# Optimization experiments

Hardware: AMD Instinct MI355X
Metric: run time of the kernel (lower is better)

Reference implementation:

```python
import jax, jax.numpy as jnp
import numpy as np

TEMP = 0.07  # temperature used as logits / 0.07 in the original


def setup_inputs() -> dict:
    key = jax.random.key(0)
    k1, k2, k3 = jax.random.split(key, 3)
    B, N, T, L, D = 8, 128, 8, 6, 256
    meta = jax.random.normal(k1, (B, N, T, L, D), dtype=jnp.float32)
    thing = jax.random.randint(k2, (B, N, T), 0, 2, dtype=jnp.int32)
    label = jax.random.randint(k3, (B, N, T), 0, 40, dtype=jnp.int32)
    return {"meta_weight_for_con": meta, "thing_gt_idx": thing, "label_tmp": label}


def _con_loss(meta, thing, label):
    # meta: [B,N,T,L,D]; thing,label: [B,N,T]
    B, N, T, L, D = meta.shape
    P = N * T
    valid = thing.reshape(B, P).astype(bool)            # [B,P] boolean gt mask
    lab = label.reshape(B, P)                           # [B,P]
    # meta_weight_b[mask] -> [K,L,D]; permute(1,0,2) -> per-layer [K,D].
    # We keep all P positions and mask instead of compacting (jit-friendly).
    w = meta.reshape(B, P, L, D).transpose(0, 2, 1, 3)  # [B,L,P,D]
    w = w / jnp.maximum(jnp.linalg.norm(w, axis=-1, keepdims=True), 1e-12)  # F.normalize
    z = jnp.einsum('blpd,blqd->blpq', w, w) / TEMP      # similarity / temp [B,L,P,P]

    same = lab[:, :, None] == lab[:, None, :]           # [B,P,P]
    vpair = valid[:, :, None] & valid[:, None, :]
    eye = jnp.eye(P, dtype=bool)
    pos_mask = same & (~eye) & vpair                    # positives: same label, not self
    neg_mask = (~same) & vpair                          # negatives: different label

    K = valid.sum(axis=1)                               # [B] ins_num_ per batch
    pos_count = pos_mask.sum(axis=-1)                   # [B,P]
    neg_count = neg_mask.sum(axis=-1)                   # [B,P]

    # --- random positive sample per (batch, layer, row), mirroring np.random.choice ---
    u = jax.random.uniform(jax.random.key(42), (B, L, P))
    r = jnp.floor(u * pos_count[:, None, :].astype(u.dtype)).astype(jnp.int32)
    r = jnp.minimum(r, jnp.maximum(pos_count - 1, 0)[:, None, :])
    ranks = jnp.cumsum(pos_mask, axis=-1) - 1           # rank of each positive in index order
    sel = pos_mask[:, None, :, :] & (ranks[:, None, :, :] == r[..., None])  # [B,L,P,P]
    zp = jnp.sum(jnp.where(sel, z, 0.0), axis=-1)       # chosen positive logit [B,L,P]
    diag = jnp.diagonal(z, axis1=-2, axis2=-1)          # self-sim fallback when no positives
    zp = jnp.where((pos_count > 0)[:, None, :], zp, diag)

    # --- last negative (original pads by repeating the last negative to K-1) ---
    iota = jnp.arange(P)
    idx_last = jnp.max(jnp.where(neg_mask, iota[None, None, :], -1), axis=-1)  # [B,P]
    idx = jnp.broadcast_to(jnp.maximum(idx_last, 0)[:, None, :, None], (B, L, P, 1))
    zl = jnp.take_along_axis(z, idx, axis=-1)[..., 0]   # [B,L,P]

    # --- stable CE with label 0: loss = lse(logits) - zp ---
    max_n = jnp.max(jnp.where(neg_mask[:, None], z, -jnp.inf), axis=-1)  # [B,L,P]
    m = jnp.maximum(zp, max_n)
    m = jnp.where(jnp.isfinite(m), m, zp)
    sum_neg = jnp.sum(jnp.where(neg_mask[:, None], jnp.exp(z - m[..., None]), 0.0), axis=-1)
    pad = jnp.maximum((K[:, None] - 1 - neg_count), 0).astype(z.dtype)   # [B,P]
    pad_term = pad[:, None, :] * jnp.where((neg_count > 0)[:, None, :], jnp.exp(zl - m), 0.0)
    loss_row = m + jnp.log(jnp.exp(zp - m) + sum_neg + pad_term) - zp    # [B,L,P]

    row_w = valid.astype(z.dtype)
    mean_per = jnp.sum(loss_row * row_w[:, None, :], axis=-1) / jnp.maximum(K, 1)[:, None].astype(z.dtype)  # [B,L]

    gate = jnp.sum((thing.sum(axis=2) > 0), axis=1) >= 2  # skip batches with <2 gt rows
    return jnp.sum(jnp.where(gate[:, None], mean_per, 0.0))


def reference(meta_weight_for_con, thing_gt_idx, label_tmp):
    return _con_loss(meta_weight_for_con, thing_gt_idx, label_tmp)
```

## Files before the change

### kernel.cpp

```cpp
#include <hip/hip_runtime.h>
#include <stdint.h>

namespace {

constexpr int Bb = 8, Ll = 6, Dd = 256, Pp = 1024;
constexpr float SCALE_Y = 14.285714285714286f * 1.4426950408889634f;
constexpr float M0y = 21.0f;
constexpr float LN2f = 0.6931471805599453f;

typedef __attribute__((ext_vector_type(4))) float floatx4;

__device__ const int PAIRS[36] = {
  0x00,0x01,0x02,0x03,0x04,0x05,0x06,0x07,
  0x11,0x12,0x13,0x14,0x15,0x16,0x17,
  0x22,0x23,0x24,0x25,0x26,0x27,
  0x33,0x34,0x35,0x36,0x37,
  0x44,0x45,0x46,0x47,
  0x55,0x56,0x57,
  0x66,0x67,
  0x77
};

__device__ __forceinline__ void async16(const void* g, void* l) {
  __builtin_amdgcn_global_load_lds(
      (const __attribute__((address_space(1))) void*)g,
      (__attribute__((address_space(3))) void*)l, 16, 0, 0);
}

__device__ __forceinline__ uint32_t rotl32(uint32_t x, int n) {
  return (x << n) | (x >> (32 - n));
}
__device__ __forceinline__ void tf_round(uint32_t& x0, uint32_t& x1, int r) {
  x0 += x1; x1 = rotl32(x1, r); x1 ^= x0;
}
__device__ void threefry2x32(uint32_t x0, uint32_t x1, uint32_t& o0, uint32_t& o1) {
  const uint32_t k0 = 0u, k1 = 42u;
  const uint32_t k2 = k0 ^ k1 ^ 0x1BD11BDAu;
  x0 += k0; x1 += k1;
  tf_round(x0,x1,13); tf_round(x0,x1,15); tf_round(x0,x1,26); tf_round(x0,x1,6);
  x0 += k1; x1 += k2 + 1u;
  tf_round(x0,x1,17); tf_round(x0,x1,29); tf_round(x0,x1,16); tf_round(x0,x1,24);
  x0 += k2; x1 += k0 + 2u;
  tf_round(x0,x1,13); tf_round(x0,x1,15); tf_round(x0,x1,26); tf_round(x0,x1,6);
  x0 += k0; x1 += k1 + 3u;
  tf_round(x0,x1,17); tf_round(x0,x1,29); tf_round(x0,x1,16); tf_round(x0,x1,24);
  x0 += k1; x1 += k2 + 4u;
  tf_round(x0,x1,13); tf_round(x0,x1,15); tf_round(x0,x1,26); tf_round(x0,x1,6);
  x0 += k2; x1 += k0 + 5u;
  o0 = x0; o1 = x1;
}
__device__ float jax_u01(uint32_t idx) {
  const uint32_t HALF = (uint32_t)(Bb * Ll * Pp / 2);
  uint32_t o0, o1, bits;
  if (idx < HALF) { threefry2x32(idx, idx + HALF, o0, o1); bits = o0; }
  else            { threefry2x32(idx - HALF, idx, o0, o1); bits = o1; }
  return __uint_as_float((bits >> 9) | 0x3f800000u) - 1.0f;
}

__device__ __forceinline__ uint32_t fp8e4m3_rne(float x) {
  uint32_t u = __float_as_uint(x);
  const uint32_t s = (u >> 24) & 0x80u;
  u &= 0x7FFFFFFFu;
  uint32_t code;
  if (u < 0x3C800000u) {
    code = (uint32_t)__float2int_rn(__uint_as_float(u) * 512.0f);
  } else {
    const uint32_t r = (u + 0x7FFFFu + ((u >> 20) & 1u)) >> 20;
    code = r - (120u << 3);
  }
  return s | code;
}
__device__ __forceinline__ float fp8e4m3_tof(uint32_t c) {
  const uint32_t e = (c >> 3) & 15u, m = c & 7u;
  float mag;
  if (e) mag = __uint_as_float(((e + 120u) << 23) | (m << 20));
  else   mag = (float)m * 0.001953125f;
  return (c & 0x80u) ? -mag : mag;
}

__device__ __forceinline__ void fp8x4_dot(uint32_t a, uint32_t b, float& s) {
#if __has_builtin(__builtin_amdgcn_cvt_f32_fp8)
  s += __builtin_amdgcn_cvt_f32_fp8((int)a, 0) * __builtin_amdgcn_cvt_f32_fp8((int)b, 0);
  s += __builtin_amdgcn_cvt_f32_fp8((int)a, 1) * __builtin_amdgcn_cvt_f32_fp8((int)b, 1);
  s += __builtin_amdgcn_cvt_f32_fp8((int)a, 2) * __builtin_amdgcn_cvt_f32_fp8((int)b, 2);
  s += __builtin_amdgcn_cvt_f32_fp8((int)a, 3) * __builtin_amdgcn_cvt_f32_fp8((int)b, 3);
#else
  s += fp8e4m3_tof(a & 0xFF) * fp8e4m3_tof(b & 0xFF);
  s += fp8e4m3_tof((a >> 8) & 0xFF) * fp8e4m3_tof((b >> 8) & 0xFF);
  s += fp8e4m3_tof((a >> 16) & 0xFF) * fp8e4m3_tof((b >> 16) & 0xFF);
  s += fp8e4m3_tof((a >> 24) & 0xFF) * fp8e4m3_tof((b >> 24) & 0xFF);
#endif
}

constexpr int NB_NORM = Bb * Pp * Ll / 4;
constexpr int NB_ROW  = Bb * Pp / 4;

__global__ void prep_k(const float* __restrict__ meta, const int* __restrict__ thing,
                       const int* __restrict__ label, uint8_t* __restrict__ wn,
                       int* __restrict__ qpos, int* __restrict__ negc,
                       int* __restrict__ qidx, int* __restrict__ Kv,
                       int* __restrict__ gatev, float* __restrict__ rowsum_g,
                       int* __restrict__ cnt2, float* __restrict__ out) {
  __shared__ int sK[256], sG[256];
  const int bid = blockIdx.x, t = threadIdx.x;

  if (bid < NB_NORM) {
    const int wid = (bid * 256 + t) >> 6;
    const int lane = t & 63;
    const float4 v = *(const float4*)(meta + (size_t)wid * Dd + lane * 4);
    float ss = v.x * v.x + v.y * v.y + v.z * v.z + v.w * v.w;
    #pragma unroll
    for (int m = 32; m; m >>= 1) ss += __shfl_xor(ss, m, 64);
    const float inv = 1.0f / fmaxf(sqrtf(ss), 1e-12f);
    const int bp = wid / Ll, l = wid - bp * Ll;
    const int b = bp >> 10, p = bp & (Pp - 1);
    uint8_t* dst = wn + ((size_t)(b * Ll + l) * Pp + p) * Dd + lane * 4;
#if __has_builtin(__builtin_amdgcn_cvt_pk_fp8_f32)
    const int lo16 = __builtin_amdgcn_cvt_pk_fp8_f32(v.x * inv, v.y * inv, 0, false);
    const uint32_t packed =
        (uint32_t)__builtin_amdgcn_cvt_pk_fp8_f32(v.z * inv, v.w * inv, lo16, true);
#else
    const uint32_t packed = fp8e4m3_rne(v.x * inv)
                          | (fp8e4m3_rne(v.y * inv) << 8)
                          | (fp8e4m3_rne(v.z * inv) << 16)
                          | (fp8e4m3_rne(v.w * inv) << 24);
#endif
    *(uint32_t*)dst = packed;
    return;
  }
  if (bid < NB_NORM + NB_ROW) {
    const int wid = (bid - NB_NORM) * 4 + (t >> 6);
    const int lane = t & 63;
    const int b = wid >> 10, p = wid & (Pp - 1);
    const int* lab = label + b * Pp;
    const int* th  = thing + b * Pp;
    const int myLab = lab[p];
    const bool myValid = (th[p] != 0);

    uint32_t posbits = 0;
    int cnt[16];
    int pc = 0, nc = 0, last = -1;
    #pragma unroll
    for (int c = 0; c < 16; ++c) {
      const int q = c * 64 + lane;
      const int lq = lab[q];
      const bool vq = (th[q] != 0);
      const bool same = (lq == myLab);
      const bool pos = myValid && vq && same && (q != p);
      const bool neg = myValid && vq && !same;
      uint64_t bp2 = __ballot(pos);
      uint64_t bn = __ballot(neg);
      if (pos) posbits |= (1u << c);
      cnt[c] = __popcll(bp2);
      pc += cnt[c];
      nc += __popcll(bn);
      if (bn) last = c * 64 + 63 - __clzll(bn);
    }
    int qsel[Ll];
    #pragma unroll
    for (int l = 0; l < Ll; ++l) qsel[l] = p;
    if (pc > 0) {
      for (int l = 0; l < Ll; ++l) {
        const float u = jax_u01((uint32_t)((b * Ll + l) * Pp + p));
        int r = (int)floorf(u * (float)pc);
        r = min(r, pc - 1);
        int base = 0;
        for (int c = 0; c < 16; ++c) {
          if (r < base + cnt[c]) {
            const bool mine = (posbits >> c) & 1u;
            uint64_t bm = __ballot(mine);
            uint64_t ltmask = (lane == 0) ? 0ull : (~0ull >> (64 - lane));
            int myrank = __popcll(bm & ltmask);
            bool hit = mine && (base + myrank == r);
            uint64_t hb = __ballot(hit);
            qsel[l] = c * 64 + (int)__builtin_ctzll(hb);
            break;
          }
          base += cnt[c];
        }
      }
    }
    if (lane == 0) {
      negc[wid] = nc;
      qidx[wid] = (last < 0) ? 0 : last;
      #pragma unroll
      for (int l = 0; l < Ll; ++l) qpos[(b * Ll + l) * Pp + p] = qsel[l];
    }
    return;
  }
  if (bid < NB_NORM + NB_ROW + Bb) {
    const int b = bid - (NB_NORM + NB_ROW);
    int k = 0;
    for (int p = t; p < Pp; p += 256) k += (thing[b * Pp + p] != 0);
    int g = 0;
    if (t < 128) {
      int any = 0;
      for (int tt = 0; tt < 8; ++tt) any |= (thing[(b * 128 + t) * 8 + tt] != 0);
      g = any;
    }
    sK[t] = k; sG[t] = g;
    __syncthreads();
    for (int s = 128; s; s >>= 1) {
      if (t < s) { sK[t] += sK[t + s]; sG[t] += sG[t + s]; }
      __syncthreads();
    }
    if (t == 0) { Kv[b] = sK[0]; gatev[b] = (sG[0] >= 2) ? 1 : 0; }
    return;
  }
  if (bid < NB_NORM + NB_ROW + Bb + 48) {
    const int zb = bid - (NB_NORM + NB_ROW + Bb);
    const int idx = zb * 256 + t;
    *(float4*)(rowsum_g + idx * 4) = (float4){0.f, 0.f, 0.f, 0.f};
    if (zb == 0 && t < 192) { cnt2[t] = 0; cnt2[t + 192] = 0; }
    return;
  }
  if (t == 0) out[0] = 0.f;
}

__global__ __launch_bounds__(256)
void gemmfinal_k(const uint8_t* __restrict__ wn,
                 const int* __restrict__ thing, const int* __restrict__ label,
                 const int* __restrict__ qpos, const int* __restrict__ qidx,
                 const int* __restrict__ negc, const int* __restrict__ Kv,
                 const int* __restrict__ gatev, float* __restrict__ rowsum_g,
                 int* __restrict__ cnt2, float* __restrict__ out) {
  __shared__ __align__(16) uint8_t As[2 * 128 * 64];
  __shared__ __align__(16) uint8_t Bs[2 * 128 * 64];
  __shared__ int labp_s[128], valp_s[128], labq_s[128], valq_s[128];
  __shared__ float rowsum_lds[128], colsum_lds[128];
  __shared__ int fin_s[2];
  __shared__ float sb[256];

  const int t = threadIdx.x;
  const int bid = blockIdx.x;
  const int xcd = bid & 7;
  const int chunk = bid >> 3;
  const int bl = xcd + 8 * (chunk % 6);
  const int b = bl / Ll;
  const int pair = PAIRS[chunk / 6];
  const int pt = pair >> 4, qt = pair & 15;
  const bool diag = (pt == qt);
  const int p0 = pt * 128, q0 = qt * 128;
  const int blP = bl * Pp;

  if (t < 128) {
    labp_s[t] = label[b * Pp + p0 + t];
    valp_s[t] = thing[b * Pp + p0 + t];
    labq_s[t] = label[b * Pp + q0 + t];
    valq_s[t] = thing[b * Pp + q0 + t];
    rowsum_lds[t] = 0.f;
    colsum_lds[t] = 0.f;
  }

  const uint8_t* Wbl = wn + (size_t)bl * Pp * Dd;
  const int lane = t & 63;
  const int w = t >> 6, wr = w >> 1, wc = w & 1;
  const int cq = lane & 15, rq = lane >> 4;
  const int wbase16 = (t & ~63) * 16;

  floatx4 acc[4][4];
  #pragma unroll
  for (int i = 0; i < 4; ++i)
    #pragma unroll
    for (int j = 0; j < 4; ++j) acc[i][j] = (floatx4){0.f, 0.f, 0.f, 0.f};

  auto STAGE = [&](int bsel, int kt) {
    const int k0 = kt * 64;
    #pragma unroll
    for (int rd = 0; rd < 2; ++rd) {
      const int c = rd * 256 + t;
      const int row = c >> 2, sp2 = c & 3;
      const int sl = sp2 ^ ((row >> 1) & 3);
      async16(Wbl + (size_t)(p0 + row) * Dd + k0 + sl * 16,
              As + bsel * 8192 + rd * 4096 + wbase16);
      if (!diag)
        async16(Wbl + (size_t)(q0 + row) * Dd + k0 + sl * 16,
                Bs + bsel * 8192 + rd * 4096 + wbase16);
    }
  };

  STAGE(0, 0);
  __syncthreads();

  const uint8_t* Bbase0 = diag ? As : Bs;
  for (int kt = 0; kt < 4; ++kt) {
    const int bsel = kt & 1;
    if (kt < 3) STAGE(bsel ^ 1, kt + 1);
    const uint8_t* Ab = As + bsel * 8192;
    const uint8_t* Bb2 = Bbase0 + bsel * 8192;
    #pragma unroll
    for (int sub = 0; sub < 2; ++sub) {
      const int Lw = sub * 2 + (rq >> 1);
      const int off8 = (rq & 1) * 8;
      long long af[4], bfr[4];
      #pragma unroll
      for (int fi = 0; fi < 4; ++fi) {
        const int row = wr * 64 + fi * 16 + cq;
        af[fi] = *(const long long*)(Ab + row * 64 + (Lw ^ ((row >> 1) & 3)) * 16 + off8);
      }
      #pragma unroll
      for (int fj = 0; fj < 4; ++fj) {
        const int row = wc * 64 + fj * 16 + cq;
        bfr[fj] = *(const long long*)(Bb2 + row * 64 + (Lw ^ ((row >> 1) & 3)) * 16 + off8);
      }
      #pragma unroll
      for (int fi = 0; fi < 4; ++fi)
        #pragma unroll
        for (int fj = 0; fj < 4; ++fj)
          acc[fi][fj] = __builtin_amdgcn_mfma_f32_16x16x32_fp8_fp8(af[fi], bfr[fj],
                                                                   acc[fi][fj], 0, 0, 0);
    }
    __syncthreads();
  }

  int qlabv[4];
  float qvalf[4];
  float csum[4] = {0.f, 0.f, 0.f, 0.f};
  #pragma unroll
  for (int fj = 0; fj < 4; ++fj) {
    const int cl = wc * 64 + fj * 16 + cq;
    qlabv[fj] = labq_s[cl];
    qvalf[fj] = valq_s[cl] ? 1.f : 0.f;
  }
  #pragma unroll
  for (int fi = 0; fi < 4; ++fi) {
    #pragma unroll
    for (int reg = 0; reg < 4; ++reg) {
      const int rl = wr * 64 + fi * 16 + rq * 4 + reg;
      const int rlab = labp_s[rl];
      const float rvalf = valp_s[rl] ? 1.f : 0.f;
      float rsum = 0.f;
      #pragma unroll
      for (int fj = 0; fj < 4; ++fj) {
        const float y = acc[fi][fj][reg] * SCALE_Y;
        const float negm = (qlabv[fj] != rlab) ? (qvalf[fj] * rvalf) : 0.f;
        const float term = negm * exp2f(y - M0y);
        rsum += term;
        csum[fj] += term;
      }
      rsum += __shfl_xor(rsum, 1); rsum += __shfl_xor(rsum, 2);
      rsum += __shfl_xor(rsum, 4); rsum += __shfl_xor(rsum, 8);
      if (cq == 0) atomicAdd(&rowsum_lds[rl], rsum);
    }
  }
  if (!diag) {
    #pragma unroll
    for (int fj = 0; fj < 4; ++fj) {
      float c = csum[fj];
      c += __shfl_xor(c, 16); c += __shfl_xor(c, 32);
      if (rq == 0) atomicAdd(&colsum_lds[wc * 64 + fj * 16 + cq], c);
    }
  }
  __syncthreads();
  if (t < 128) {
    atomicAdd(&rowsum_g[blP + p0 + t], rowsum_lds[t]);
    if (!diag) atomicAdd(&rowsum_g[blP + q0 + t], colsum_lds[t]);
  }
  __syncthreads();

  if (t == 0) {
    const int n1 = __hip_atomic_fetch_add(&cnt2[bl * 8 + pt], 1,
                                          __ATOMIC_RELAXED, __HIP_MEMORY_SCOPE_AGENT);
    fin_s[0] = (n1 == 7);
    int f1 = 0;
    if (!diag) {
      const int n2 = __hip_atomic_fetch_add(&cnt2[bl * 8 + qt], 1,
                                            __ATOMIC_RELAXED, __HIP_MEMORY_SCOPE_AGENT);
      f1 = (n2 == 7);
    }
    fin_s[1] = f1;
  }
  __syncthreads();

  float accl = 0.f;
  if ((fin_s[0] | fin_s[1]) && gatev[b]) {
    const int Kb = Kv[b];
    const float invK = 1.f / (float)max(Kb, 1);
    const int half = t & 1;
    const int rrow = t >> 1;
    #pragma unroll
    for (int fr = 0; fr < 2; ++fr) {
      if (!fin_s[fr]) continue;
      const int p = (fr ? qt : pt) * 128 + rrow;
      const int valid = thing[b * Pp + p];
      const int qp = qpos[blP + p];
      const int qi = qidx[b * Pp + p];
      const uint8_t* rp = Wbl + (size_t)p  * Dd + half * 128;
      const uint8_t* rq2 = Wbl + (size_t)qp * Dd + half * 128;
      const uint8_t* rx = Wbl + (size_t)qi * Dd + half * 128;
      float sp = 0.f, sl = 0.f;
      #pragma unroll
      for (int i = 0; i < 8; ++i) {
        const uint4 a4 = *(const uint4*)(rp + i * 16);
        const uint4 b4 = *(const uint4*)(rq2 + i * 16);
        const uint4 c4 = *(const uint4*)(rx + i * 16);
        fp8x4_dot(a4.x, b4.x, sp); fp8x4_dot(a4.y, b4.y, sp);
        fp8x4_dot(a4.z, b4.z, sp); fp8x4_dot(a4.w, b4.w, sp);
        fp8x4_dot(a4.x, c4.x, sl); fp8x4_dot(a4.y, c4.y, sl);
        fp8x4_dot(a4.z, c4.z, sl); fp8x4_dot(a4.w, c4.w, sl);
      }
      sp += __shfl_xor(sp, 1);
      sl += __shfl_xor(sl, 1);
      if (half == 0 && valid != 0) {
        const float yp = sp * SCALE_Y, yl = sl * SCALE_Y;
        const float rs = __hip_atomic_load(&rowsum_g[blP + p],
                                           __ATOMIC_RELAXED, __HIP_MEMORY_SCOPE_AGENT);
        const int nc = negc[b * Pp + p];
        const float pad = fmaxf((float)(Kb - 1 - nc), 0.f);
        const float tot = exp2f(yp - M0y) + rs + ((nc > 0) ? pad * exp2f(yl - M0y) : 0.f);
        accl += LN2f * (M0y + log2f(tot) - yp) * invK;
      }
    }
  }
  sb[t] = accl;
  __syncthreads();
  for (int s = 128; s; s >>= 1) {
    if (t < s) sb[t] += sb[t + s];
    __syncthreads();
  }
  if (t == 0 && sb[0] != 0.f) atomicAdd(out, sb[0]);
}

}

extern "C" void kernel_launch(void* const* d_in, const int* in_sizes, int n_in,
                              void* d_out, int out_size, void* d_ws, size_t ws_size,
                              hipStream_t stream) {
  const float* meta = (const float*)d_in[0];
  const int* thing  = (const int*)d_in[1];
  const int* label  = (const int*)d_in[2];
  float* out = (float*)d_out;

  char* ws = (char*)d_ws;
  size_t off = 0;
  uint8_t* wn = (uint8_t*)(ws + off); off += (size_t)Bb * Ll * Pp * Dd;
  int* qpos  = (int*)(ws + off); off += (size_t)Bb * Ll * Pp * 4;
  int* negc  = (int*)(ws + off); off += (size_t)Bb * Pp * 4;
  int* qidx  = (int*)(ws + off); off += (size_t)Bb * Pp * 4;
  int* Kv    = (int*)(ws + off); off += 64;
  int* gatev = (int*)(ws + off); off += 64;
  float* rowsum_g = (float*)(ws + off); off += (size_t)Bb * Ll * Pp * 4;
  int* cnt2  = (int*)(ws + off); off += 384 * 4;

  const int nb_prep = NB_NORM + NB_ROW + Bb + 48 + 1;
  prep_k<<<nb_prep, 256, 0, stream>>>(meta, thing, label, wn, qpos, negc, qidx,
                                      Kv, gatev, rowsum_g, cnt2, out);
  gemmfinal_k<<<8 * 6 * 36, 256, 0, stream>>>(wn, thing, label, qpos, qidx, negc,
                                              Kv, gatev, rowsum_g, cnt2, out);
}
```

Measured before the change: 148.9 us.

## Double threads per GEMM block to 512 with 2x4 wave tiling

The fused GEMM+epilogue kernel now runs 512 threads (8 waves) per block, each wave computing a 64x32 sub-tile instead of 64x64. This halves accumulator registers per wave and raises the number of waves resident per CU, aiming to hide LDS and global latency better. Staging, the final row-dot phase (now split four ways per row) and the block reduction are adjusted to match. The exp argument is also folded into an fma. The cost is more block-wide barrier traffic and less data reuse per wave.

```diff
diff --git a/kernel.cpp b/kernel.cpp
--- a/kernel.cpp
+++ b/kernel.cpp
@@ -217,7 +217,7 @@
   if (t == 0) out[0] = 0.f;
 }
 
-__global__ __launch_bounds__(256)
+__global__ __launch_bounds__(512, 6)
 void gemmfinal_k(const uint8_t* __restrict__ wn,
                  const int* __restrict__ thing, const int* __restrict__ label,
                  const int* __restrict__ qpos, const int* __restrict__ qidx,
@@ -229,7 +229,7 @@
   __shared__ int labp_s[128], valp_s[128], labq_s[128], valq_s[128];
   __shared__ float rowsum_lds[128], colsum_lds[128];
   __shared__ int fin_s[2];
-  __shared__ float sb[256];
+  __shared__ float sb[512];
 
   const int t = threadIdx.x;
   const int bid = blockIdx.x;
@@ -254,29 +254,26 @@
 
   const uint8_t* Wbl = wn + (size_t)bl * Pp * Dd;
   const int lane = t & 63;
-  const int w = t >> 6, wr = w >> 1, wc = w & 1;
+  const int w = t >> 6;
+  const int wr = w >> 2, wc = w & 3;
   const int cq = lane & 15, rq = lane >> 4;
   const int wbase16 = (t & ~63) * 16;
 
-  floatx4 acc[4][4];
+  floatx4 acc[4][2];
   #pragma unroll
   for (int i = 0; i < 4; ++i)
     #pragma unroll
-    for (int j = 0; j < 4; ++j) acc[i][j] = (floatx4){0.f, 0.f, 0.f, 0.f};
+    for (int j = 0; j < 2; ++j) acc[i][j] = (floatx4){0.f, 0.f, 0.f, 0.f};
 
   auto STAGE = [&](int bsel, int kt) {
     const int k0 = kt * 64;
-    #pragma unroll
-    for (int rd = 0; rd < 2; ++rd) {
-      const int c = rd * 256 + t;
-      const int row = c >> 2, sp2 = c & 3;
-      const int sl = sp2 ^ ((row >> 1) & 3);
-      async16(Wbl + (size_t)(p0 + row) * Dd + k0 + sl * 16,
-              As + bsel * 8192 + rd * 4096 + wbase16);
-      if (!diag)
-        async16(Wbl + (size_t)(q0 + row) * Dd + k0 + sl * 16,
-                Bs + bsel * 8192 + rd * 4096 + wbase16);
-    }
+    const int row = t >> 2, sp2 = t & 3;
+    const int sl = sp2 ^ ((row >> 1) & 3);
+    async16(Wbl + (size_t)(p0 + row) * Dd + k0 + sl * 16,
+            As + bsel * 8192 + wbase16);
+    if (!diag)
+      async16(Wbl + (size_t)(q0 + row) * Dd + k0 + sl * 16,
+              Bs + bsel * 8192 + wbase16);
   };
 
   STAGE(0, 0);
@@ -292,33 +289,33 @@
     for (int sub = 0; sub < 2; ++sub) {
       const int Lw = sub * 2 + (rq >> 1);
       const int off8 = (rq & 1) * 8;
-      long long af[4], bfr[4];
+      long long af[4], bfr[2];
       #pragma unroll
       for (int fi = 0; fi < 4; ++fi) {
         const int row = wr * 64 + fi * 16 + cq;
         af[fi] = *(const long long*)(Ab + row * 64 + (Lw ^ ((row >> 1) & 3)) * 16 + off8);
       }
       #pragma unroll
-      for (int fj = 0; fj < 4; ++fj) {
-        const int row = wc * 64 + fj * 16 + cq;
+      for (int fj = 0; fj < 2; ++fj) {
+        const int row = wc * 32 + fj * 16 + cq;
         bfr[fj] = *(const long long*)(Bb2 + row * 64 + (Lw ^ ((row >> 1) & 3)) * 16 + off8);
       }
       #pragma unroll
       for (int fi = 0; fi < 4; ++fi)
         #pragma unroll
-        for (int fj = 0; fj < 4; ++fj)
+        for (int fj = 0; fj < 2; ++fj)
           acc[fi][fj] = __builtin_amdgcn_mfma_f32_16x16x32_fp8_fp8(af[fi], bfr[fj],
                                                                    acc[fi][fj], 0, 0, 0);
     }
     __syncthreads();
   }
 
-  int qlabv[4];
-  float qvalf[4];
-  float csum[4] = {0.f, 0.f, 0.f, 0.f};
+  int qlabv[2];
+  float qvalf[2];
+  float csum[2] = {0.f, 0.f};
   #pragma unroll
-  for (int fj = 0; fj < 4; ++fj) {
-    const int cl = wc * 64 + fj * 16 + cq;
+  for (int fj = 0; fj < 2; ++fj) {
+    const int cl = wc * 32 + fj * 16 + cq;
     qlabv[fj] = labq_s[cl];
     qvalf[fj] = valq_s[cl] ? 1.f : 0.f;
   }
@@ -331,10 +328,10 @@
       const float rvalf = valp_s[rl] ? 1.f : 0.f;
       float rsum = 0.f;
       #pragma unroll
-      for (int fj = 0; fj < 4; ++fj) {
-        const float y = acc[fi][fj][reg] * SCALE_Y;
+      for (int fj = 0; fj < 2; ++fj) {
+        const float e = exp2f(fmaf(acc[fi][fj][reg], SCALE_Y, -M0y));
         const float negm = (qlabv[fj] != rlab) ? (qvalf[fj] * rvalf) : 0.f;
-        const float term = negm * exp2f(y - M0y);
+        const float term = negm * e;
         rsum += term;
         csum[fj] += term;
       }
@@ -345,10 +342,10 @@
   }
   if (!diag) {
     #pragma unroll
-    for (int fj = 0; fj < 4; ++fj) {
+    for (int fj = 0; fj < 2; ++fj) {
       float c = csum[fj];
       c += __shfl_xor(c, 16); c += __shfl_xor(c, 32);
-      if (rq == 0) atomicAdd(&colsum_lds[wc * 64 + fj * 16 + cq], c);
+      if (rq == 0) atomicAdd(&colsum_lds[wc * 32 + fj * 16 + cq], c);
     }
   }
   __syncthreads();
@@ -376,8 +373,8 @@
   if ((fin_s[0] | fin_s[1]) && gatev[b]) {
     const int Kb = Kv[b];
     const float invK = 1.f / (float)max(Kb, 1);
-    const int half = t & 1;
-    const int rrow = t >> 1;
+    const int qtr = t & 3;
+    const int rrow = t >> 2;
     #pragma unroll
     for (int fr = 0; fr < 2; ++fr) {
       if (!fin_s[fr]) continue;
@@ -385,12 +382,12 @@
       const int valid = thing[b * Pp + p];
       const int qp = qpos[blP + p];
       const int qi = qidx[b * Pp + p];
-      const uint8_t* rp = Wbl + (size_t)p  * Dd + half * 128;
-      const uint8_t* rq2 = Wbl + (size_t)qp * Dd + half * 128;
-      const uint8_t* rx = Wbl + (size_t)qi * Dd + half * 128;
+      const uint8_t* rp = Wbl + (size_t)p  * Dd + qtr * 64;
+      const uint8_t* rq2 = Wbl + (size_t)qp * Dd + qtr * 64;
+      const uint8_t* rx = Wbl + (size_t)qi * Dd + qtr * 64;
       float sp = 0.f, sl = 0.f;
       #pragma unroll
-      for (int i = 0; i < 8; ++i) {
+      for (int i = 0; i < 4; ++i) {
         const uint4 a4 = *(const uint4*)(rp + i * 16);
         const uint4 b4 = *(const uint4*)(rq2 + i * 16);
         const uint4 c4 = *(const uint4*)(rx + i * 16);
@@ -399,9 +396,9 @@
         fp8x4_dot(a4.x, c4.x, sl); fp8x4_dot(a4.y, c4.y, sl);
         fp8x4_dot(a4.z, c4.z, sl); fp8x4_dot(a4.w, c4.w, sl);
       }
-      sp += __shfl_xor(sp, 1);
-      sl += __shfl_xor(sl, 1);
-      if (half == 0 && valid != 0) {
+      sp += __shfl_xor(sp, 1); sp += __shfl_xor(sp, 2);
+      sl += __shfl_xor(sl, 1); sl += __shfl_xor(sl, 2);
+      if (qtr == 0 && valid != 0) {
         const float yp = sp * SCALE_Y, yl = sl * SCALE_Y;
         const float rs = __hip_atomic_load(&rowsum_g[blP + p],
                                            __ATOMIC_RELAXED, __HIP_MEMORY_SCOPE_AGENT);
@@ -414,7 +411,7 @@
   }
   sb[t] = accl;
   __syncthreads();
-  for (int s = 128; s; s >>= 1) {
+  for (int s = 256; s; s >>= 1) {
     if (t < s) sb[t] += sb[t + s];
     __syncthreads();
   }
@@ -445,6 +442,6 @@
   const int nb_prep = NB_NORM + NB_ROW + Bb + 48 + 1;
   prep_k<<<nb_prep, 256, 0, stream>>>(meta, thing, label, wn, qpos, negc, qidx,
                                       Kv, gatev, rowsum_g, cnt2, out);
-  gemmfinal_k<<<8 * 6 * 36, 256, 0, stream>>>(wn, thing, label, qpos, qidx, negc,
+  gemmfinal_k<<<8 * 6 * 36, 512, 0, stream>>>(wn, thing, label, qpos, qidx, negc,
                                               Kv, gatev, rowsum_g, cnt2, out);
 }
```

Result: no change. 149.6 us (+0.4%).
